# Performance work log

Measured on AMD Instinct MI355X. Metric: run time of the kernel, lower is better.

## Reference

```python
import jax, jax.numpy as jnp
import numpy as np

EPS_F = 1e-12
M, N = 64, 4096  # feature dim m, num nodes n


def setup_inputs() -> dict:
    key = jax.random.key(0)
    k1, k2, k3, k4 = jax.random.split(key, 4)
    # X: (m, n) node features transposed, as in the repo (features.t())
    X = jax.random.normal(k1, (M, N), dtype=jnp.float32)
    # F: (m, m) parameter, xavier_uniform init
    bound = float(np.sqrt(6.0 / (M + M)))
    F = jax.random.uniform(k2, (M, M), minval=-bound, maxval=bound, dtype=jnp.float32)
    # Q_S: (n, n) orthogonal eigenvector matrix of the (symmetric, normalized) adjacency
    A = jax.random.normal(k3, (N, N), dtype=jnp.float32)
    Q_S, _ = jnp.linalg.qr(A)
    Q_S = Q_S.astype(jnp.float32)
    # Lambda_S: (n, 1) eigenvalues of normalized adjacency, inside (-1, 1)
    Lambda_S = jnp.sort(
        jax.random.uniform(k4, (N, 1), minval=-0.95, maxval=0.95, dtype=jnp.float32), axis=0
    )
    gamma = jnp.asarray(0.8, dtype=jnp.float32)
    return {"X": X, "F": F, "Q_S": Q_S, "Lambda_S": Lambda_S, "gamma": gamma}


def reference(X, F, Q_S, Lambda_S, gamma):
    # g(F) = F^T F / (||F^T F||_F + eps)  -- Frobenius-normalized Gram matrix
    FF = F.T @ F                                   # (m, m)
    G_F = FF / (jnp.linalg.norm(FF) + EPS_F)       # (m, m), symmetric PSD, ||.||_F ~ 1
    # spectral decomposition of g(F)
    Lambda_F, Q_F = jnp.linalg.eigh(G_F)           # (m,), (m, m)
    # closed-form equilibrium of Z = gamma * g(F) Z S^T + X in the joint eigenbasis
    D = 1.0 / (1.0 - gamma * Lambda_F[:, None] * Lambda_S.reshape(1, -1))  # (m, n)
    Z = Q_F @ (D * (Q_F.T @ X @ Q_S)) @ Q_S.T      # (m, n)
    return Z
```

## Files before the change

kernel.cpp:

```cpp
#include <hip/hip_runtime.h>
#include <math.h>


typedef short short8 __attribute__((ext_vector_type(8)));
typedef float floatx16 __attribute__((ext_vector_type(16)));

#define KSPLIT 16
#define KCHUNK 256
constexpr int Mdim = 64;
constexpr int Ndim = 4096;
constexpr int TILE = Mdim * Ndim;

__device__ inline ushort f2bf(float f) {
    uint u = __float_as_uint(f);
    u += 0x7fff + ((u >> 16) & 1);
    return (ushort)(u >> 16);
}
__device__ inline float bf2f(ushort h) { return __uint_as_float(((uint)h) << 16); }

__device__ inline floatx16 mfma_bf16(short8 a, short8 b, floatx16 c) {
    return __builtin_amdgcn_mfma_f32_32x32x16_bf16(a, b, c, 0, 0, 0);
}

union SharedG1 {
    struct { ushort Ah[4096], Al[4096], Bh[4096]; } g;
    struct { ushort planes[2][4096]; float red[256]; } p;
};

__device__ inline void barrier_nodrain() {
    asm volatile("s_waitcnt lgkmcnt(0)" ::: "memory");
    __builtin_amdgcn_s_barrier();
    __builtin_amdgcn_sched_barrier(0);
}

__device__ void prep_body(SharedG1& sh, const float* __restrict__ F, float* __restrict__ Gout) {
    const int t = threadIdx.x;
    const int l = t & 63, w = t >> 6;
    const int tm = w & 1, tn = w >> 1;
    const int am = tm * 32 + (l & 31);
    const int bn = tn * 32 + (l & 31);
    const int lk = l >> 5;
    ushort* Ph = sh.p.planes[0];
    ushort* Pl = sh.p.planes[1];
    float* red = sh.p.red;

    {
        const int r = t >> 2, c0 = (t & 3) * 16;
#pragma unroll
        for (int q = 0; q < 4; ++q) {
            float4 v = *(const float4*)&F[r * 64 + c0 + 4 * q];
            float fa[4] = {v.x, v.y, v.z, v.w};
#pragma unroll
            for (int i = 0; i < 4; ++i) {
                int c = c0 + 4 * q + i;
                ushort h = f2bf(fa[i]);
                int idx = c * 64 + (((r >> 3) ^ (c & 7)) * 8) + (r & 7);
                Ph[idx] = h;
                Pl[idx] = f2bf(fa[i] - bf2f(h));
            }
        }
    }
    barrier_nodrain();
    floatx16 acc;
    for (int i = 0; i < 16; ++i) acc[i] = 0.f;
    for (int s16 = 0; s16 < 4; ++s16) {
        int gk = 2 * s16 + lk;
        int ai = am * 64 + ((gk ^ (am & 7)) * 8);
        int bi = bn * 64 + ((gk ^ (bn & 7)) * 8);
        short8 ah = *(const short8*)&Ph[ai];
        short8 al = *(const short8*)&Pl[ai];
        short8 bh = *(const short8*)&Ph[bi];
        short8 bl = *(const short8*)&Pl[bi];
        acc = mfma_bf16(ah, bh, acc);
        acc = mfma_bf16(al, bh, acc);
        acc = mfma_bf16(ah, bl, acc);
    }
    float ss = 0.f;
    for (int r = 0; r < 16; ++r) ss += acc[r] * acc[r];
    red[t] = ss;
    barrier_nodrain();
    for (int off = 128; off > 0; off >>= 1) {
        if (t < off) red[t] += red[t + off];
        barrier_nodrain();
    }
    const float inv = 1.0f / (sqrtf(red[0]) + 1e-12f);
    for (int r = 0; r < 16; ++r) {
        int row = (r & 3) + 8 * (r >> 2) + 4 * lk + tm * 32;
        int col = tn * 32 + (l & 31);
        float v = acc[r] * inv;
        Gout[row * 64 + col] = v;
        ushort h = f2bf(v);
        int idx = row * 64 + (((col >> 3) ^ (row & 7)) * 8 + (col & 7));
        Ph[idx] = h;
        Pl[idx] = f2bf(v - bf2f(h));
    }
    for (int j = 1; j < 5; ++j) {
        barrier_nodrain();
        floatx16 a2;
        for (int i = 0; i < 16; ++i) a2[i] = 0.f;
        for (int s16 = 0; s16 < 4; ++s16) {
            int gk = 2 * s16 + lk;
            int ai = am * 64 + ((gk ^ (am & 7)) * 8);
            int bi = bn * 64 + ((gk ^ (bn & 7)) * 8);
            short8 ah = *(const short8*)&Ph[ai];
            short8 al = *(const short8*)&Pl[ai];
            short8 bh = *(const short8*)&Ph[bi];
            short8 bl = *(const short8*)&Pl[bi];
            a2 = mfma_bf16(ah, bh, a2);
            a2 = mfma_bf16(al, bh, a2);
            a2 = mfma_bf16(ah, bl, a2);
        }
        barrier_nodrain();
        for (int r = 0; r < 16; ++r) {
            int row = (r & 3) + 8 * (r >> 2) + 4 * lk + tm * 32;
            int col = tn * 32 + (l & 31);
            float v = a2[r];
            Gout[j * 4096 + row * 64 + col] = v;
            ushort h = f2bf(v);
            int idx = row * 64 + (((col >> 3) ^ (row & 7)) * 8 + (col & 7));
            Ph[idx] = h;
            Pl[idx] = f2bf(v - bf2f(h));
        }
    }
}

template <bool TB>
__device__ inline void load_b(float4 (&dst)[4], const float* __restrict__ Bm,
                              int n0, int kk, int sr, int sj, int nq, int kr2) {
    if constexpr (TB) {
#pragma unroll
        for (int s = 0; s < 4; ++s)
            dst[s] = *(const float4*)&Bm[(size_t)(n0 + sr) * 4096 + kk + 4 * sj + 16 * s];
    } else {
#pragma unroll
        for (int s = 0; s < 2; ++s) {
            dst[2 * s + 0] = *(const float4*)&Bm[(size_t)(kk + kr2 + 32 * s) * 4096 + n0 + 4 * nq];
            dst[2 * s + 1] = *(const float4*)&Bm[(size_t)(kk + kr2 + 1 + 32 * s) * 4096 + n0 + 4 * nq];
        }
    }
}

__global__ __launch_bounds__(256, 4) void gemm1_kernel(const float* __restrict__ A,
                                                       const float* __restrict__ Bm,
                                                       float* __restrict__ C,
                                                       const float* __restrict__ F,
                                                       float* __restrict__ Gp) {
    __shared__ SharedG1 sh;
    const int bid = blockIdx.x;
    if (bid == 0) { prep_body(sh, F, Gp); return; }
    const int b = bid - 1;
    const int nt = b & 63;
    const int n0 = nt * 64;
    const int ks = b >> 6;
    const int kb = ks * KCHUNK;
    const int t = threadIdx.x;
    const int l = t & 63, w = t >> 6;
    const int tm = w & 1, tn = w >> 1;
    const int am = tm * 32 + (l & 31);
    const int bn = tn * 32 + (l & 31);
    const int lk = l >> 5;
    const int sr = t >> 2, sj = t & 3;
    const int nq = t & 15, kr2 = 2 * (t >> 4);

    floatx16 acc;
    for (int i = 0; i < 16; ++i) acc[i] = 0.f;

    float4 bbuf[4][4];
    load_b<false>(bbuf[0], Bm, n0, kb, sr, sj, nq, kr2);
    load_b<false>(bbuf[1], Bm, n0, kb + 64, sr, sj, nq, kr2);

#pragma unroll
    for (int step = 0; step < KCHUNK / 64; ++step) {
        const int k0 = kb + step * 64;
        float4 av[4];
#pragma unroll
        for (int s = 0; s < 4; ++s)
            av[s] = *(const float4*)&A[sr * 4096 + k0 + 4 * sj + 16 * s];
        if (step + 2 < KCHUNK / 64)
            load_b<false>(bbuf[step + 2], Bm, n0, k0 + 128, sr, sj, nq, kr2);
        barrier_nodrain();
#pragma unroll
        for (int s = 0; s < 2; ++s) {
            int k = kr2 + 32 * s;
            float fa[4] = {bbuf[step][2 * s].x, bbuf[step][2 * s].y, bbuf[step][2 * s].z, bbuf[step][2 * s].w};
            float fb[4] = {bbuf[step][2 * s + 1].x, bbuf[step][2 * s + 1].y, bbuf[step][2 * s + 1].z, bbuf[step][2 * s + 1].w};
#pragma unroll
            for (int i = 0; i < 4; ++i) {
                int n = 4 * nq + i;
                int idx = n * 64 + (((k >> 3) ^ (n & 7)) * 8 + (k & 7));
                ushort2 hp2;
                hp2.x = f2bf(fa[i]);
                hp2.y = f2bf(fb[i]);
                *(ushort2*)&sh.g.Bh[idx] = hp2;
            }
        }
#pragma unroll
        for (int s = 0; s < 4; ++s) {
            int off = 4 * sj + 16 * s;
            int idx = sr * 64 + (((off >> 3) ^ (sr & 7)) * 8 + (off & 7));
            float fa[4] = {av[s].x, av[s].y, av[s].z, av[s].w};
            ushort4 h4, l4;
            ushort* hp = (ushort*)&h4; ushort* lp = (ushort*)&l4;
#pragma unroll
            for (int i = 0; i < 4; ++i) {
                ushort h = f2bf(fa[i]);
                hp[i] = h; lp[i] = f2bf(fa[i] - bf2f(h));
            }
            *(ushort4*)&sh.g.Ah[idx] = h4;
            *(ushort4*)&sh.g.Al[idx] = l4;
        }
        barrier_nodrain();
#pragma unroll
        for (int s16 = 0; s16 < 4; ++s16) {
            int gk = 2 * s16 + lk;
            int ai = am * 64 + ((gk ^ (am & 7)) * 8);
            int bi = bn * 64 + ((gk ^ (bn & 7)) * 8);
            short8 ah = *(const short8*)&sh.g.Ah[ai];
            short8 al = *(const short8*)&sh.g.Al[ai];
            short8 bh = *(const short8*)&sh.g.Bh[bi];
            acc = mfma_bf16(ah, bh, acc);
            acc = mfma_bf16(al, bh, acc);
        }
    }
    float* Cp = C + (size_t)ks * TILE + nt * 4096;
    const int base = w * 1024 + l;
#pragma unroll
    for (int r = 0; r < 16; ++r) Cp[base + r * 64] = acc[r];
}

__global__ __launch_bounds__(256) void reduce_kernel(const float* __restrict__ P,
                                                     float* __restrict__ out) {
    const int i = blockIdx.x * 256 + threadIdx.x;
    float4 a = {0.f, 0.f, 0.f, 0.f};
#pragma unroll
    for (int s = 0; s < KSPLIT; ++s) {
        const float4 v = *(const float4*)&P[(size_t)s * TILE + 4 * i];
        a.x += v.x; a.y += v.y; a.z += v.z; a.w += v.w;
    }
    *(float4*)&out[4 * i] = a;
}

__global__ __launch_bounds__(256) void solve_kernel(const float* __restrict__ W,
                                                    const float* __restrict__ Gp,
                                                    const float* __restrict__ lam,
                                                    const float* __restrict__ gammap,
                                                    ushort* __restrict__ Yh,
                                                    ushort* __restrict__ Yl) {
    __shared__ float Gs[64][68];
    __shared__ float T[64][17];
    const int t = threadIdx.x;
    const int c0 = blockIdx.x * 16;
    const int nt = blockIdx.x >> 2;
    for (int e = t; e < 1024; e += 256) {
        const int row = e >> 4, cc = e & 15;
        const int cit = (blockIdx.x & 3) * 16 + cc;
        const int rr = (row & 3) | (((row >> 3) & 3) << 2);
        const int lk = (row >> 2) & 1;
        const int ww = (row >> 5) + 2 * (cit >> 5);
        const int ll = (cit & 31) + 32 * lk;
        T[row][cc] = W[nt * 4096 + ww * 1024 + rr * 64 + ll];
    }
    const int tx = t & 15;
    const int r4 = (t >> 4) * 4;
    const float a0 = gammap[0] * lam[c0 + tx];
    float s = a0;
    for (int j = 0; j < 5; ++j) {
        __syncthreads();
        for (int e = t; e < 4096; e += 256) Gs[e >> 6][e & 63] = Gp[j * 4096 + e];
        __syncthreads();
        float u0 = 0.f, u1 = 0.f, u2 = 0.f, u3 = 0.f;
#pragma unroll 8
        for (int k = 0; k < 64; ++k) {
            const float tv = T[k][tx];
            const float4 g = *(const float4*)&Gs[k][r4];
            u0 += g.x * tv; u1 += g.y * tv; u2 += g.z * tv; u3 += g.w * tv;
        }
        __syncthreads();
        T[r4 + 0][tx] += s * u0;
        T[r4 + 1][tx] += s * u1;
        T[r4 + 2][tx] += s * u2;
        T[r4 + 3][tx] += s * u3;
        s = s * s;
    }
    __syncthreads();
    for (int e = t; e < 1024; e += 256) {
        const int r = e >> 4, cc = e & 15, col = c0 + cc;
        const float v = T[r][cc];
        const ushort h = f2bf(v);
        const int idx = (col >> 3) * 512 + r * 8 + (col & 7);
        Yh[idx] = h;
        Yl[idx] = f2bf(v - bf2f(h));
    }
}

__global__ __launch_bounds__(256, 4) void gemm2_kernel(const ushort* __restrict__ Yh,
                                                       const ushort* __restrict__ Yl,
                                                       const float* __restrict__ Bm,
                                                       float* __restrict__ C) {
    __shared__ ushort Bhs[2][4096];
    const int b = blockIdx.x;
    const int nt = b & 63;
    const int n0 = nt * 64;
    const int ks = b >> 6;
    const int kb = ks * KCHUNK;
    const int t = threadIdx.x;
    const int l = t & 63, w = t >> 6;
    const int tm = w & 1, tn = w >> 1;
    const int am = tm * 32 + (l & 31);
    const int bn = tn * 32 + (l & 31);
    const int lk = l >> 5;
    const int sr = t >> 2, sj = t & 3;

    floatx16 acc;
    for (int i = 0; i < 16; ++i) acc[i] = 0.f;

    float4 bbuf[4][4];
#pragma unroll
    for (int st = 0; st < 4; ++st)
        load_b<true>(bbuf[st], Bm, n0, kb + 64 * st, sr, sj, 0, 0);

#pragma unroll
    for (int step = 0; step < KCHUNK / 64; ++step) {
        const int k0 = kb + step * 64;
        const int par = step & 1;
        short8 afh[4], afl[4];
#pragma unroll
        for (int s16 = 0; s16 < 4; ++s16) {
            int gk = (k0 >> 3) + 2 * s16 + lk;
            afh[s16] = *(const short8*)&Yh[gk * 512 + am * 8];
            afl[s16] = *(const short8*)&Yl[gk * 512 + am * 8];
        }
#pragma unroll
        for (int s = 0; s < 4; ++s) {
            int off = 4 * sj + 16 * s;
            int idx = sr * 64 + (((off >> 3) ^ (sr & 7)) * 8 + (off & 7));
            float fb[4] = {bbuf[step][s].x, bbuf[step][s].y, bbuf[step][s].z, bbuf[step][s].w};
            ushort4 h4;
            ushort* hp = (ushort*)&h4;
#pragma unroll
            for (int i = 0; i < 4; ++i) hp[i] = f2bf(fb[i]);
            *(ushort4*)&Bhs[par][idx] = h4;
        }
        barrier_nodrain();
#pragma unroll
        for (int s16 = 0; s16 < 4; ++s16) {
            int gk = 2 * s16 + lk;
            int bi = bn * 64 + ((gk ^ (bn & 7)) * 8);
            short8 bh = *(const short8*)&Bhs[par][bi];
            acc = mfma_bf16(afh[s16], bh, acc);
            acc = mfma_bf16(afl[s16], bh, acc);
        }
    }
    float* Cp = C + (size_t)ks * TILE + nt * 4096;
    const int base = w * 1024 + l;
#pragma unroll
    for (int r = 0; r < 16; ++r) Cp[base + r * 64] = acc[r];
}

__global__ __launch_bounds__(256) void reduce2z_kernel(const float* __restrict__ P,
                                                       float* __restrict__ Z) {
    __shared__ float a4[2][8][64];
    const int bid = blockIdx.x;
    const int nt = bid & 63;
    const int q = bid >> 6;
    const int tm = q >> 1;
    const int rbase = (q & 1) * 8;
    const int t = threadIdx.x;
    const int tn = t >> 7, rr = (t >> 4) & 7, lq = t & 15;
    const size_t off = (size_t)nt * 4096 + (tm + 2 * tn) * 1024 + (rbase + rr) * 64 + 4 * lq;
    float4 a = {0.f, 0.f, 0.f, 0.f};
#pragma unroll
    for (int s = 0; s < KSPLIT; ++s) {
        const float4 v = *(const float4*)&P[(size_t)s * TILE + off];
        a.x += v.x; a.y += v.y; a.z += v.z; a.w += v.w;
    }
    *(float4*)&a4[tn][rr][4 * lq] = a;
    __syncthreads();
    const int orow = q * 16 + (t >> 4);
    const int cquad = t & 15;
    const int lk = (orow >> 2) & 1;
    const int rr2 = ((orow & 3) | (((orow >> 3) & 3) << 2)) - rbase;
    float4 o;
    float* op = (float*)&o;
#pragma unroll
    for (int v = 0; v < 4; ++v) {
        const int col = 4 * cquad + v;
        op[v] = a4[col >> 5][rr2][(col & 31) + 32 * lk];
    }
    *(float4*)&Z[(size_t)orow * 4096 + nt * 64 + 4 * cquad] = o;
}

extern "C" void kernel_launch(void* const* d_in, const int* in_sizes, int n_in,
                              void* d_out, int out_size, void* d_ws, size_t ws_size,
                              hipStream_t stream) {
    const float* X     = (const float*)d_in[0];
    const float* F     = (const float*)d_in[1];
    const float* Qs    = (const float*)d_in[2];
    const float* lam   = (const float*)d_in[3];
    const float* gamma = (const float*)d_in[4];
    float* Z = (float*)d_out;

    float* P1 = (float*)d_ws;
    float* P2 = P1 + (size_t)KSPLIT * TILE;
    float* W  = P2 + (size_t)KSPLIT * TILE;
    float* Gp = W + TILE;
    ushort* Yh = (ushort*)(Gp + 5 * 4096);
    ushort* Yl = Yh + TILE;

    gemm1_kernel<<<64 * KSPLIT + 1, 256, 0, stream>>>(X, Qs, P1, F, Gp);
    reduce_kernel<<<256, 256, 0, stream>>>(P1, W);
    solve_kernel<<<Ndim / 16, 256, 0, stream>>>(W, Gp, lam, gamma, Yh, Yl);
    gemm2_kernel<<<64 * KSPLIT, 256, 0, stream>>>(Yh, Yl, Qs, P2);
    reduce2z_kernel<<<256, 256, 0, stream>>>(P2, Z);
}
```

Measured before the change: 160.2 us.

## Pre-pack Q_S into swizzled bf16 tiles shared by both GEMMs

Adds a pack kernel that converts Q_S to bf16 once and writes two pre-swizzled tile layouts, a normal one and a transposed one. Both GEMMs then copy contiguous 16-byte chunks straight into shared memory instead of loading fp32 and converting and scattering per element. This halves the bytes read for Q_S in each GEMM and removes the conversion and scatter work from the inner loops. In exchange it adds a separate pass that reads all of Q_S in fp32 and writes two bf16 copies, plus an extra kernel launch.

```diff
diff --git a/kernel.cpp b/kernel.cpp
--- a/kernel.cpp
+++ b/kernel.cpp
@@ -31,6 +31,49 @@
     asm volatile("s_waitcnt lgkmcnt(0)" ::: "memory");
     __builtin_amdgcn_s_barrier();
     __builtin_amdgcn_sched_barrier(0);
+}
+
+__global__ __launch_bounds__(256, 4) void pack_kernel(const float* __restrict__ Qs,
+                                                      ushort* __restrict__ QN,
+                                                      ushort* __restrict__ QT) {
+    __shared__ ushort Ls[64][264];
+    const int b = blockIdx.x;
+    const int bt = b >> 4;
+    const int cq = b & 15;
+    const int t = threadIdx.x;
+    const int r = t >> 2, j = t & 3;
+    const float* src = Qs + (size_t)(64 * bt + r) * 4096 + 256 * cq;
+#pragma unroll
+    for (int it = 0; it < 16; ++it) {
+        float4 v = *(const float4*)&src[16 * it + 4 * j];
+        ushort4 h;
+        h.x = f2bf(v.x); h.y = f2bf(v.y); h.z = f2bf(v.z); h.w = f2bf(v.w);
+        *(ushort4*)&Ls[r][16 * it + 4 * j] = h;
+    }
+    __syncthreads();
+    const int n = t >> 2;
+#pragma unroll
+    for (int i = 0; i < 4; ++i) {
+        ushort* pl = QN + ((size_t)bt * 64 + 4 * cq + i) * 4096;
+#pragma unroll
+        for (int gg = 0; gg < 2; ++gg) {
+            int g = 2 * (t & 3) + gg;
+            uint4 v = *(const uint4*)&Ls[n][64 * i + 8 * g];
+            *(uint4*)&pl[n * 64 + ((g ^ (n & 7)) * 8)] = v;
+        }
+    }
+#pragma unroll
+    for (int i = 0; i < 4; ++i) {
+        ushort* pl = QT + ((size_t)(4 * cq + i) * 64 + bt) * 4096;
+#pragma unroll
+        for (int gg = 0; gg < 2; ++gg) {
+            int g = 2 * (t & 3) + gg;
+            short8 w;
+#pragma unroll
+            for (int u = 0; u < 8; ++u) w[u] = (short)Ls[8 * g + u][64 * i + n];
+            *(short8*)&pl[n * 64 + ((g ^ (n & 7)) * 8)] = w;
+        }
+    }
 }
 
 __device__ void prep_body(SharedG1& sh, const float* __restrict__ F, float* __restrict__ Gout) {
@@ -124,24 +167,8 @@
     }
 }
 
-template <bool TB>
-__device__ inline void load_b(float4 (&dst)[4], const float* __restrict__ Bm,
-                              int n0, int kk, int sr, int sj, int nq, int kr2) {
-    if constexpr (TB) {
-#pragma unroll
-        for (int s = 0; s < 4; ++s)
-            dst[s] = *(const float4*)&Bm[(size_t)(n0 + sr) * 4096 + kk + 4 * sj + 16 * s];
-    } else {
-#pragma unroll
-        for (int s = 0; s < 2; ++s) {
-            dst[2 * s + 0] = *(const float4*)&Bm[(size_t)(kk + kr2 + 32 * s) * 4096 + n0 + 4 * nq];
-            dst[2 * s + 1] = *(const float4*)&Bm[(size_t)(kk + kr2 + 1 + 32 * s) * 4096 + n0 + 4 * nq];
-        }
-    }
-}
-
 __global__ __launch_bounds__(256, 4) void gemm1_kernel(const float* __restrict__ A,
-                                                       const float* __restrict__ Bm,
+                                                       const ushort* __restrict__ QT,
                                                        float* __restrict__ C,
                                                        const float* __restrict__ F,
                                                        float* __restrict__ Gp) {
@@ -150,7 +177,6 @@
     if (bid == 0) { prep_body(sh, F, Gp); return; }
     const int b = bid - 1;
     const int nt = b & 63;
-    const int n0 = nt * 64;
     const int ks = b >> 6;
     const int kb = ks * KCHUNK;
     const int t = threadIdx.x;
@@ -160,14 +186,13 @@
     const int bn = tn * 32 + (l & 31);
     const int lk = l >> 5;
     const int sr = t >> 2, sj = t & 3;
-    const int nq = t & 15, kr2 = 2 * (t >> 4);
 
     floatx16 acc;
     for (int i = 0; i < 16; ++i) acc[i] = 0.f;
 
-    float4 bbuf[4][4];
-    load_b<false>(bbuf[0], Bm, n0, kb, sr, sj, nq, kr2);
-    load_b<false>(bbuf[1], Bm, n0, kb + 64, sr, sj, nq, kr2);
+    const ushort* qtb = QT + ((size_t)nt * 64 + 4 * ks) * 4096;
+    uint4 bc0 = *(const uint4*)&qtb[(size_t)t * 8];
+    uint4 bc1 = *(const uint4*)&qtb[2048 + (size_t)t * 8];
 
 #pragma unroll
     for (int step = 0; step < KCHUNK / 64; ++step) {
@@ -176,24 +201,14 @@
 #pragma unroll
         for (int s = 0; s < 4; ++s)
             av[s] = *(const float4*)&A[sr * 4096 + k0 + 4 * sj + 16 * s];
-        if (step + 2 < KCHUNK / 64)
-            load_b<false>(bbuf[step + 2], Bm, n0, k0 + 128, sr, sj, nq, kr2);
-        barrier_nodrain();
-#pragma unroll
-        for (int s = 0; s < 2; ++s) {
-            int k = kr2 + 32 * s;
-            float fa[4] = {bbuf[step][2 * s].x, bbuf[step][2 * s].y, bbuf[step][2 * s].z, bbuf[step][2 * s].w};
-            float fb[4] = {bbuf[step][2 * s + 1].x, bbuf[step][2 * s + 1].y, bbuf[step][2 * s + 1].z, bbuf[step][2 * s + 1].w};
-#pragma unroll
-            for (int i = 0; i < 4; ++i) {
-                int n = 4 * nq + i;
-                int idx = n * 64 + (((k >> 3) ^ (n & 7)) * 8 + (k & 7));
-                ushort2 hp2;
-                hp2.x = f2bf(fa[i]);
-                hp2.y = f2bf(fb[i]);
-                *(ushort2*)&sh.g.Bh[idx] = hp2;
-            }
-        }
+        uint4 bn0, bn1;
+        if (step + 1 < KCHUNK / 64) {
+            bn0 = *(const uint4*)&qtb[(size_t)(step + 1) * 4096 + t * 8];
+            bn1 = *(const uint4*)&qtb[(size_t)(step + 1) * 4096 + 2048 + t * 8];
+        }
+        barrier_nodrain();
+        *(uint4*)&sh.g.Bh[t * 8] = bc0;
+        *(uint4*)&sh.g.Bh[2048 + t * 8] = bc1;
 #pragma unroll
         for (int s = 0; s < 4; ++s) {
             int off = 4 * sj + 16 * s;
@@ -221,6 +236,7 @@
             acc = mfma_bf16(ah, bh, acc);
             acc = mfma_bf16(al, bh, acc);
         }
+        bc0 = bn0; bc1 = bn1;
     }
     float* Cp = C + (size_t)ks * TILE + nt * 4096;
     const int base = w * 1024 + l;
@@ -295,12 +311,11 @@
 
 __global__ __launch_bounds__(256, 4) void gemm2_kernel(const ushort* __restrict__ Yh,
                                                        const ushort* __restrict__ Yl,
-                                                       const float* __restrict__ Bm,
+                                                       const ushort* __restrict__ QN,
                                                        float* __restrict__ C) {
     __shared__ ushort Bhs[2][4096];
     const int b = blockIdx.x;
     const int nt = b & 63;
-    const int n0 = nt * 64;
     const int ks = b >> 6;
     const int kb = ks * KCHUNK;
     const int t = threadIdx.x;
@@ -309,20 +324,23 @@
     const int am = tm * 32 + (l & 31);
     const int bn = tn * 32 + (l & 31);
     const int lk = l >> 5;
-    const int sr = t >> 2, sj = t & 3;
 
     floatx16 acc;
     for (int i = 0; i < 16; ++i) acc[i] = 0.f;
 
-    float4 bbuf[4][4];
-#pragma unroll
-    for (int st = 0; st < 4; ++st)
-        load_b<true>(bbuf[st], Bm, n0, kb + 64 * st, sr, sj, 0, 0);
+    const ushort* qnb = QN + ((size_t)nt * 64 + 4 * ks) * 4096;
+    uint4 bc0 = *(const uint4*)&qnb[(size_t)t * 8];
+    uint4 bc1 = *(const uint4*)&qnb[2048 + (size_t)t * 8];
 
 #pragma unroll
     for (int step = 0; step < KCHUNK / 64; ++step) {
         const int k0 = kb + step * 64;
         const int par = step & 1;
+        uint4 bn0, bn1;
+        if (step + 1 < KCHUNK / 64) {
+            bn0 = *(const uint4*)&qnb[(size_t)(step + 1) * 4096 + t * 8];
+            bn1 = *(const uint4*)&qnb[(size_t)(step + 1) * 4096 + 2048 + t * 8];
+        }
         short8 afh[4], afl[4];
 #pragma unroll
         for (int s16 = 0; s16 < 4; ++s16) {
@@ -330,17 +348,8 @@
             afh[s16] = *(const short8*)&Yh[gk * 512 + am * 8];
             afl[s16] = *(const short8*)&Yl[gk * 512 + am * 8];
         }
-#pragma unroll
-        for (int s = 0; s < 4; ++s) {
-            int off = 4 * sj + 16 * s;
-            int idx = sr * 64 + (((off >> 3) ^ (sr & 7)) * 8 + (off & 7));
-            float fb[4] = {bbuf[step][s].x, bbuf[step][s].y, bbuf[step][s].z, bbuf[step][s].w};
-            ushort4 h4;
-            ushort* hp = (ushort*)&h4;
-#pragma unroll
-            for (int i = 0; i < 4; ++i) hp[i] = f2bf(fb[i]);
-            *(ushort4*)&Bhs[par][idx] = h4;
-        }
+        *(uint4*)&Bhs[par][t * 8] = bc0;
+        *(uint4*)&Bhs[par][2048 + t * 8] = bc1;
         barrier_nodrain();
 #pragma unroll
         for (int s16 = 0; s16 < 4; ++s16) {
@@ -350,6 +359,7 @@
             acc = mfma_bf16(afh[s16], bh, acc);
             acc = mfma_bf16(afl[s16], bh, acc);
         }
+        bc0 = bn0; bc1 = bn1;
     }
     float* Cp = C + (size_t)ks * TILE + nt * 4096;
     const int base = w * 1024 + l;
@@ -406,10 +416,13 @@
     float* Gp = W + TILE;
     ushort* Yh = (ushort*)(Gp + 5 * 4096);
     ushort* Yl = Yh + TILE;
-
-    gemm1_kernel<<<64 * KSPLIT + 1, 256, 0, stream>>>(X, Qs, P1, F, Gp);
+    ushort* QT = Yl + TILE;
+    ushort* QN = QT + (size_t)64 * 64 * 4096;
+
+    pack_kernel<<<1024, 256, 0, stream>>>(Qs, QN, QT);
+    gemm1_kernel<<<64 * KSPLIT + 1, 256, 0, stream>>>(X, QT, P1, F, Gp);
     reduce_kernel<<<256, 256, 0, stream>>>(P1, W);
     solve_kernel<<<Ndim / 16, 256, 0, stream>>>(W, Gp, lam, gamma, Yh, Yl);
-    gemm2_kernel<<<64 * KSPLIT, 256, 0, stream>>>(Yh, Yl, Qs, P2);
+    gemm2_kernel<<<64 * KSPLIT, 256, 0, stream>>>(Yh, Yl, QN, P2);
     reduce2z_kernel<<<256, 256, 0, stream>>>(P2, Z);
 }
```

Result: slower. 179.0 us (+11.7%).
